# Kernel tuning notes

Hardware: AMD Instinct MI355X
Metric: run time of the kernel (lower is better)

The kernel has to match this reference:

```python
import jax, jax.numpy as jnp
import numpy as np

N_TOTAL = 1_048_576   # total points across all clouds
B = 4096              # number of point clouds
IN_FEATURES = 4
POINT_DIMS = [4, 64, 128, 256, 256]   # point encoding: 3 Linear+LeakyReLU, then final Linear(256,256)
LATENT_DIMS = [256, 256, 256]         # latent encoding: 2 Linear+LeakyReLU
LATENT_DIM = 256


def _linear_params(key, fan_in, fan_out):
    # torch nn.Linear default init: U(-1/sqrt(fan_in), 1/sqrt(fan_in))
    k1, k2 = jax.random.split(key)
    lim = 1.0 / np.sqrt(fan_in)
    w = jax.random.uniform(k1, (fan_out, fan_in), minval=-lim, maxval=lim, dtype=jnp.float32)
    b = jax.random.uniform(k2, (fan_out,), minval=-lim, maxval=lim, dtype=jnp.float32)
    return w, b


def setup_inputs() -> dict:
    key = jax.random.key(0)
    keys = jax.random.split(key, 16)
    inp = {}
    inp["points"] = jax.random.normal(keys[0], (N_TOTAL, IN_FEATURES), dtype=jnp.float32)
    # cumulative segment ends; even partition so no segment is empty (avg 256 pts/cloud)
    inp["idx"] = (jnp.arange(1, B + 1, dtype=jnp.int32) * N_TOTAL) // B
    # point encoding params
    inp["pw0"], inp["pb0"] = _linear_params(keys[1], POINT_DIMS[0], POINT_DIMS[1])
    inp["pw1"], inp["pb1"] = _linear_params(keys[2], POINT_DIMS[1], POINT_DIMS[2])
    inp["pw2"], inp["pb2"] = _linear_params(keys[3], POINT_DIMS[2], POINT_DIMS[3])
    inp["pw3"], inp["pb3"] = _linear_params(keys[4], POINT_DIMS[3], POINT_DIMS[4])
    # latent encoding params
    inp["lw0"], inp["lb0"] = _linear_params(keys[5], LATENT_DIMS[0], LATENT_DIMS[1])
    inp["lw1"], inp["lb1"] = _linear_params(keys[6], LATENT_DIMS[1], LATENT_DIMS[2])
    # mu / logvar heads
    inp["mw"], inp["mb"] = _linear_params(keys[7], LATENT_DIMS[2], LATENT_DIM)
    inp["vw"], inp["vb"] = _linear_params(keys[8], LATENT_DIMS[2], LATENT_DIM)
    return inp


def reference(points, idx, pw0, pb0, pw1, pb1, pw2, pb2, pw3, pb3,
              lw0, lb0, lw1, lb1, mw, mb, vw, vb):
    lrelu = jax.nn.leaky_relu  # default negative_slope=0.01, same as torch LeakyReLU
    h = lrelu(points @ pw0.T + pb0)
    h = lrelu(h @ pw1.T + pb1)
    h = lrelu(h @ pw2.T + pb2)
    h = h @ pw3.T + pb3                          # [N, 256]
    n = h.shape[0]
    b = idx.shape[0]
    # segment id of each point: i s.t. idx[i-1] <= j < idx[i]
    seg = jnp.searchsorted(idx, jnp.arange(n, dtype=idx.dtype), side="right")
    sums = jax.ops.segment_sum(h, seg, num_segments=b)            # [B, 256]
    counts = idx - jnp.concatenate([jnp.zeros((1,), idx.dtype), idx[:-1]])
    latent = sums / counts[:, None].astype(h.dtype)               # per-cloud mean
    # latent encoding
    latent = lrelu(latent @ lw0.T + lb0)
    latent = lrelu(latent @ lw1.T + lb1)
    mu = latent @ mw.T + mb
    log_var = latent @ vw.T + vb
    return mu, log_var
```

## Files before the change

### kernel.cpp

```cpp
#include <hip/hip_runtime.h>


#define NB    4096
#define NTOT  1048576
#define PTS   64
#define OUT_HALF (NB * 256)
#define WSPLIT_ELEMS 106496

typedef __attribute__((ext_vector_type(8))) short short8;
typedef __attribute__((ext_vector_type(4))) float f32x4;
typedef unsigned short u16;
typedef unsigned int   u32;

__device__ __forceinline__ float lrelu(float x){ return x > 0.0f ? x : 0.01f * x; }

__device__ __forceinline__ u16 f2bf(float x){
  union{float f; u32 u;} v; v.f = x;
  u32 r = v.u + 0x7fffu + ((v.u >> 16) & 1u);
  return (u16)(r >> 16);
}
__device__ __forceinline__ float bf2f(u16 h){
  union{u32 u; float f;} v; v.u = ((u32)h) << 16; return v.f;
}

__device__ __forceinline__ int find_cloud(const int* __restrict__ idx, int j){
  int lo = 0, hi = NB;
  while (lo < hi){
    int mid = (lo + hi) >> 1;
    if (idx[mid] <= j) lo = mid + 1; else hi = mid;
  }
  return lo;
}

__global__ void wsplit_kernel(const float* __restrict__ w1,
                              const float* __restrict__ w2,
                              const float* __restrict__ w3,
                              u16* __restrict__ Whi, u16* __restrict__ Wlo){
  const int tid = blockIdx.x * 256 + threadIdx.x;
  const float* W; int K, off;
  if (tid < 8192)       { W = w1; K = 64;  off = 0; }
  else if (tid < 40960) { W = w2; K = 128; off = 8192; }
  else                  { W = w3; K = 256; off = 40960; }
  const int t      = tid - off;
  const int fragId = t >> 9;
  const int r      = t & 511;
  const int lane   = r >> 3, e = r & 7;
  const int KS     = K / 32;
  const int ks     = fragId % KS, mtg = fragId / KS;
  const int m      = mtg * 16 + (lane & 15);
  const int k      = ks * 32 + (lane >> 4) * 8 + e;
  const float v = W[(size_t)m * K + k];
  const u16 hi = f2bf(v);
  const u16 lo = f2bf(v - bf2f(hi));
  Whi[tid] = hi; Wlo[tid] = lo;
}

template<int K, int M, int LDSKI, int LDSKO, bool WRITE>
__device__ __forceinline__ void mfma_layer(
    const u16* __restrict__ hin, u16* __restrict__ hout,
    const u16* __restrict__ Whi, const u16* __restrict__ Wlo,
    const float* __restrict__ bias, int w, int lane, f32x4 (*__restrict__ accRet)[4])
{
  constexpr int KS  = K / 32;
  constexpr int MTW = M / 64;
  const int lrow = lane & 15;
  const int g    = lane >> 4;

  f32x4 acc[4][MTW];
  #pragma unroll
  for (int mt = 0; mt < MTW; ++mt){
    const float bv = bias[(w * MTW + mt) * 16 + lrow];
    #pragma unroll
    for (int a = 0; a < 4; ++a){
      acc[a][mt][0] = bv; acc[a][mt][1] = bv; acc[a][mt][2] = bv; acc[a][mt][3] = bv;
    }
  }
  #pragma unroll
  for (int ks = 0; ks < KS; ++ks){
    const int eoff = ks * 32 + g * 8;
    short8 af[4];
    #pragma unroll
    for (int a = 0; a < 4; ++a)
      af[a] = *reinterpret_cast<const short8*>(hin + (a * 16 + lrow) * LDSKI + eoff);
    #pragma unroll
    for (int mt = 0; mt < MTW; ++mt){
      const int fragId = (w * MTW + mt) * KS + ks;
      const short8 bh = *reinterpret_cast<const short8*>(Whi + fragId * 512 + lane * 8);
      const short8 bl = *reinterpret_cast<const short8*>(Wlo + fragId * 512 + lane * 8);
      #pragma unroll
      for (int a = 0; a < 4; ++a)
        acc[a][mt] = __builtin_amdgcn_mfma_f32_16x16x32_bf16(af[a], bh, acc[a][mt], 0, 0, 0);
      #pragma unroll
      for (int a = 0; a < 4; ++a)
        acc[a][mt] = __builtin_amdgcn_mfma_f32_16x16x32_bf16(af[a], bl, acc[a][mt], 0, 0, 0);
    }
  }
  if constexpr (WRITE){
    #pragma unroll
    for (int a = 0; a < 4; ++a)
      #pragma unroll
      for (int mt = 0; mt < MTW; ++mt){
        const int m = (w * MTW + mt) * 16 + lrow;
        #pragma unroll
        for (int r = 0; r < 4; ++r){
          const int pt = a * 16 + g * 4 + r;
          hout[pt * LDSKO + m] = f2bf(lrelu(acc[a][mt][r]));
        }
      }
  } else {
    #pragma unroll
    for (int a = 0; a < 4; ++a)
      #pragma unroll
      for (int mt = 0; mt < MTW; ++mt)
        accRet[a][mt] = acc[a][mt];
  }
}

__global__ __launch_bounds__(256, 2)
void point_mfma_kernel(const float* __restrict__ points, const int* __restrict__ idx,
    const float* __restrict__ w0, const float* __restrict__ b0,
    const float* __restrict__ b1, const float* __restrict__ b2,
    const float* __restrict__ b3,
    const u16* __restrict__ Whi, const u16* __restrict__ Wlo,
    float* __restrict__ sums)
{
  __shared__ u16 h1[PTS][72];
  __shared__ u16 h2[PTS][136];
  __shared__ u16 h3[PTS][264];

  const int t    = threadIdx.x;
  const int base = blockIdx.x * PTS;
  const int w    = t >> 6;
  const int lane = t & 63;

  {
    const int pt  = t & 63;
    const int grp = t >> 6;
    const float4 pv = *reinterpret_cast<const float4*>(points + (size_t)(base + pt) * 4);
    #pragma unroll
    for (int j = 0; j < 16; ++j){
      const int m = grp * 16 + j;
      const float4 wv = *reinterpret_cast<const float4*>(w0 + m * 4);
      const float s = b0[m] + pv.x * wv.x + pv.y * wv.y + pv.z * wv.z + pv.w * wv.w;
      h1[pt][m] = f2bf(lrelu(s));
    }
  }
  __syncthreads();
  mfma_layer< 64, 128,  72, 136, true >(&h1[0][0], &h2[0][0], Whi + 0,     Wlo + 0,     b1, w, lane, nullptr);
  __syncthreads();
  mfma_layer<128, 256, 136, 264, true >(&h2[0][0], &h3[0][0], Whi + 8192,  Wlo + 8192,  b2, w, lane, nullptr);
  __syncthreads();
  f32x4 acc3[4][4];
  mfma_layer<256, 256, 264,   1, false>(&h3[0][0], nullptr,   Whi + 40960, Wlo + 40960, b3, w, lane, acc3);

  const int lrow = lane & 15;
  const int cF = find_cloud(idx, base);
  const int cL = find_cloud(idx, base + PTS - 1);
  if (cF == cL){
    #pragma unroll
    for (int mt = 0; mt < 4; ++mt){
      float s = 0.0f;
      #pragma unroll
      for (int a = 0; a < 4; ++a){
        const f32x4 v = acc3[a][mt];
        s += v[0] + v[1] + v[2] + v[3];
      }
      s += __shfl_xor(s, 16, 64);
      s += __shfl_xor(s, 32, 64);
      if (lane < 16)
        atomicAdd(sums + (size_t)cF * 256 + (w * 4 + mt) * 16 + lrow, s);
    }
  } else {
    const int g = lane >> 4;
    #pragma unroll
    for (int a = 0; a < 4; ++a)
      #pragma unroll
      for (int mt = 0; mt < 4; ++mt)
        #pragma unroll
        for (int r = 0; r < 4; ++r){
          const int pt = base + a * 16 + g * 4 + r;
          const int c  = find_cloud(idx, pt);
          atomicAdd(sums + (size_t)c * 256 + (w * 4 + mt) * 16 + lrow, acc3[a][mt][r]);
        }
  }
}

__device__ __forceinline__ void lat_accum(const float (*__restrict__ in)[256],
    const float* __restrict__ W, const float* __restrict__ bias, int t, float acc[4])
{
  const float bv = bias[t];
  #pragma unroll
  for (int cl = 0; cl < 4; ++cl) acc[cl] = bv;
  const float4* __restrict__ wrow = reinterpret_cast<const float4*>(W + (size_t)t * 256);
  #pragma unroll 4
  for (int k4 = 0; k4 < 64; ++k4){
    const float4 w = wrow[k4];
    #pragma unroll
    for (int cl = 0; cl < 4; ++cl){
      const float4 a = *reinterpret_cast<const float4*>(&in[cl][k4 * 4]);
      acc[cl] += a.x * w.x + a.y * w.y + a.z * w.z + a.w * w.w;
    }
  }
}

__global__ __launch_bounds__(256)
void latent_kernel(const float* __restrict__ sums, const int* __restrict__ idx,
    const float* __restrict__ lw0, const float* __restrict__ lb0,
    const float* __restrict__ lw1, const float* __restrict__ lb1,
    const float* __restrict__ mw, const float* __restrict__ mb,
    const float* __restrict__ vw, const float* __restrict__ vb,
    float* __restrict__ out)
{
  __shared__ float s_in[4][256];
  __shared__ float s_a[4][256];
  const int t  = threadIdx.x;
  const int c0 = blockIdx.x * 4;

  #pragma unroll
  for (int cl = 0; cl < 4; ++cl){
    const int c = c0 + cl;
    const int cnt = idx[c] - (c ? idx[c - 1] : 0);
    s_in[cl][t] = sums[(size_t)c * 256 + t] / (float)cnt;
  }
  __syncthreads();

  float acc[4];
  lat_accum(s_in, lw0, lb0, t, acc);
  #pragma unroll
  for (int cl = 0; cl < 4; ++cl) s_a[cl][t] = lrelu(acc[cl]);
  __syncthreads();

  lat_accum(s_a, lw1, lb1, t, acc);
  __syncthreads();
  #pragma unroll
  for (int cl = 0; cl < 4; ++cl) s_in[cl][t] = lrelu(acc[cl]);
  __syncthreads();

  float accm[4], accv[4];
  lat_accum(s_in, mw, mb, t, accm);
  lat_accum(s_in, vw, vb, t, accv);
  #pragma unroll
  for (int cl = 0; cl < 4; ++cl){
    out[(size_t)(c0 + cl) * 256 + t]                    = accm[cl];
    out[(size_t)OUT_HALF + (size_t)(c0 + cl) * 256 + t] = accv[cl];
  }
}

extern "C" void kernel_launch(void* const* d_in, const int* in_sizes, int n_in,
                              void* d_out, int out_size, void* d_ws, size_t ws_size,
                              hipStream_t stream) {
  const float* points = (const float*)d_in[0];
  const int*   idx    = (const int*)  d_in[1];
  const float* pw0 = (const float*)d_in[2],  *pb0 = (const float*)d_in[3];
  const float* pw1 = (const float*)d_in[4],  *pb1 = (const float*)d_in[5];
  const float* pw2 = (const float*)d_in[6],  *pb2 = (const float*)d_in[7];
  const float* pw3 = (const float*)d_in[8],  *pb3 = (const float*)d_in[9];
  const float* lw0 = (const float*)d_in[10], *lb0 = (const float*)d_in[11];
  const float* lw1 = (const float*)d_in[12], *lb1 = (const float*)d_in[13];
  const float* mw  = (const float*)d_in[14], *mb  = (const float*)d_in[15];
  const float* vw  = (const float*)d_in[16], *vb  = (const float*)d_in[17];
  float* out  = (float*)d_out;

  const size_t sums_bytes = (size_t)NB * 256 * sizeof(float);
  const size_t wsplit_bytes = (size_t)WSPLIT_ELEMS * 2;
  float* sums; u16* Whi; u16* Wlo;
  if (ws_size >= sums_bytes + 2 * wsplit_bytes){
    sums = (float*)d_ws;
    Whi  = (u16*)((char*)d_ws + sums_bytes);
    Wlo  = Whi + WSPLIT_ELEMS;
  } else {
    Whi  = (u16*)d_out;
    Wlo  = Whi + WSPLIT_ELEMS;
    sums = out + OUT_HALF;
  }

  hipMemsetAsync(sums, 0, sums_bytes, stream);
  wsplit_kernel<<<WSPLIT_ELEMS / 256, 256, 0, stream>>>(pw1, pw2, pw3, Whi, Wlo);
  point_mfma_kernel<<<NTOT / PTS, 256, 0, stream>>>(points, idx,
      pw0, pb0, pb1, pb2, pb3, Whi, Wlo, sums);
  latent_kernel<<<NB / 4, 256, 0, stream>>>(sums, idx,
      lw0, lb0, lw1, lb1, mw, mb, vw, vb, out);
}
```

Measured before the change: 1.166 ms.

## Alias LDS buffers, batch weight loads, raise occupancy, widen latent blocks

The point kernel now overlays the h1 and h3 LDS buffers in one shared array and raises its launch-bounds minimum from 2 to 3 blocks per CU, aiming to cut LDS and register pressure so more blocks stay resident. The MFMA inner loop is reordered to loop over output tiles first and to load up to four hi/lo weight fragments at once before issuing the MFMAs, which hides global-load latency. The latent kernel handles 16 clouds per block instead of 4, so each weight row is read once for four times as many clouds. The risks are register spills under the tighter launch bound, activation fragments now being reloaded from LDS once per output tile, and fewer latent blocks to spread across the GPU.

Result: faster. 1.084 ms (-7.1%).

```diff
diff --git a/kernel.cpp b/kernel.cpp
--- a/kernel.cpp
+++ b/kernel.cpp
@@ -51,8 +51,8 @@
   const int k      = ks * 32 + (lane >> 4) * 8 + e;
   const float v = W[(size_t)m * K + k];
   const u16 hi = f2bf(v);
-  const u16 lo = f2bf(v - bf2f(hi));
-  Whi[tid] = hi; Wlo[tid] = lo;
+  Whi[tid] = hi;
+  Wlo[tid] = f2bf(v - bf2f(hi));
 }
 
 template<int K, int M, int LDSKI, int LDSKO, bool WRITE>
@@ -63,6 +63,7 @@
 {
   constexpr int KS  = K / 32;
   constexpr int MTW = M / 64;
+  constexpr int KC  = (KS < 4) ? KS : 4;
   const int lrow = lane & 15;
   const int g    = lane >> 4;
 
@@ -75,26 +76,38 @@
       acc[a][mt][0] = bv; acc[a][mt][1] = bv; acc[a][mt][2] = bv; acc[a][mt][3] = bv;
     }
   }
-  #pragma unroll
-  for (int ks = 0; ks < KS; ++ks){
-    const int eoff = ks * 32 + g * 8;
-    short8 af[4];
-    #pragma unroll
-    for (int a = 0; a < 4; ++a)
-      af[a] = *reinterpret_cast<const short8*>(hin + (a * 16 + lrow) * LDSKI + eoff);
-    #pragma unroll
-    for (int mt = 0; mt < MTW; ++mt){
-      const int fragId = (w * MTW + mt) * KS + ks;
-      const short8 bh = *reinterpret_cast<const short8*>(Whi + fragId * 512 + lane * 8);
-      const short8 bl = *reinterpret_cast<const short8*>(Wlo + fragId * 512 + lane * 8);
-      #pragma unroll
-      for (int a = 0; a < 4; ++a)
-        acc[a][mt] = __builtin_amdgcn_mfma_f32_16x16x32_bf16(af[a], bh, acc[a][mt], 0, 0, 0);
-      #pragma unroll
-      for (int a = 0; a < 4; ++a)
-        acc[a][mt] = __builtin_amdgcn_mfma_f32_16x16x32_bf16(af[a], bl, acc[a][mt], 0, 0, 0);
-    }
-  }
+
+  const u16* __restrict__ bptr = Whi + (size_t)(w * MTW) * KS * 512 + lane * 8;
+  const u16* __restrict__ lptr = Wlo + (size_t)(w * MTW) * KS * 512 + lane * 8;
+
+  #pragma unroll
+  for (int mt = 0; mt < MTW; ++mt){
+    #pragma unroll
+    for (int kc = 0; kc < KS; kc += KC){
+      short8 bh[KC], bl[KC];
+      #pragma unroll
+      for (int i = 0; i < KC; ++i){
+        bh[i] = *reinterpret_cast<const short8*>(bptr + (size_t)(mt * KS + kc + i) * 512);
+        bl[i] = *reinterpret_cast<const short8*>(lptr + (size_t)(mt * KS + kc + i) * 512);
+      }
+      #pragma unroll
+      for (int i = 0; i < KC; ++i){
+        const int ks = kc + i;
+        short8 af[4];
+        const int eoff = ks * 32 + g * 8;
+        #pragma unroll
+        for (int a = 0; a < 4; ++a)
+          af[a] = *reinterpret_cast<const short8*>(hin + (a * 16 + lrow) * LDSKI + eoff);
+        #pragma unroll
+        for (int a = 0; a < 4; ++a)
+          acc[a][mt] = __builtin_amdgcn_mfma_f32_16x16x32_bf16(af[a], bh[i], acc[a][mt], 0, 0, 0);
+        #pragma unroll
+        for (int a = 0; a < 4; ++a)
+          acc[a][mt] = __builtin_amdgcn_mfma_f32_16x16x32_bf16(af[a], bl[i], acc[a][mt], 0, 0, 0);
+      }
+    }
+  }
+
   if constexpr (WRITE){
     #pragma unroll
     for (int a = 0; a < 4; ++a)
@@ -116,7 +129,7 @@
   }
 }
 
-__global__ __launch_bounds__(256, 2)
+__global__ __launch_bounds__(256, 3)
 void point_mfma_kernel(const float* __restrict__ points, const int* __restrict__ idx,
     const float* __restrict__ w0, const float* __restrict__ b0,
     const float* __restrict__ b1, const float* __restrict__ b2,
@@ -124,9 +137,10 @@
     const u16* __restrict__ Whi, const u16* __restrict__ Wlo,
     float* __restrict__ sums)
 {
-  __shared__ u16 h1[PTS][72];
-  __shared__ u16 h2[PTS][136];
-  __shared__ u16 h3[PTS][264];
+  __shared__ __align__(16) char smem[51200];
+  u16 (*h2)[136] = reinterpret_cast<u16(*)[136]>(smem);
+  u16 (*h1)[72]  = reinterpret_cast<u16(*)[72]>(smem + 17408);
+  u16 (*h3)[264] = reinterpret_cast<u16(*)[264]>(smem + 17408);
 
   const int t    = threadIdx.x;
   const int base = blockIdx.x * PTS;
@@ -185,18 +199,19 @@
   }
 }
 
+#define CPB 16
 __device__ __forceinline__ void lat_accum(const float (*__restrict__ in)[256],
-    const float* __restrict__ W, const float* __restrict__ bias, int t, float acc[4])
+    const float* __restrict__ W, const float* __restrict__ bias, int t, float* acc)
 {
   const float bv = bias[t];
   #pragma unroll
-  for (int cl = 0; cl < 4; ++cl) acc[cl] = bv;
+  for (int cl = 0; cl < CPB; ++cl) acc[cl] = bv;
   const float4* __restrict__ wrow = reinterpret_cast<const float4*>(W + (size_t)t * 256);
   #pragma unroll 4
   for (int k4 = 0; k4 < 64; ++k4){
     const float4 w = wrow[k4];
     #pragma unroll
-    for (int cl = 0; cl < 4; ++cl){
+    for (int cl = 0; cl < CPB; ++cl){
       const float4 a = *reinterpret_cast<const float4*>(&in[cl][k4 * 4]);
       acc[cl] += a.x * w.x + a.y * w.y + a.z * w.z + a.w * w.w;
     }
@@ -211,36 +226,36 @@
     const float* __restrict__ vw, const float* __restrict__ vb,
     float* __restrict__ out)
 {
-  __shared__ float s_in[4][256];
-  __shared__ float s_a[4][256];
+  __shared__ float s_in[CPB][256];
+  __shared__ float s_a[CPB][256];
   const int t  = threadIdx.x;
-  const int c0 = blockIdx.x * 4;
-
-  #pragma unroll
-  for (int cl = 0; cl < 4; ++cl){
+  const int c0 = blockIdx.x * CPB;
+
+  #pragma unroll
+  for (int cl = 0; cl < CPB; ++cl){
     const int c = c0 + cl;
     const int cnt = idx[c] - (c ? idx[c - 1] : 0);
     s_in[cl][t] = sums[(size_t)c * 256 + t] / (float)cnt;
   }
   __syncthreads();
 
-  float acc[4];
+  float acc[CPB];
   lat_accum(s_in, lw0, lb0, t, acc);
   #pragma unroll
-  for (int cl = 0; cl < 4; ++cl) s_a[cl][t] = lrelu(acc[cl]);
+  for (int cl = 0; cl < CPB; ++cl) s_a[cl][t] = lrelu(acc[cl]);
   __syncthreads();
 
   lat_accum(s_a, lw1, lb1, t, acc);
   __syncthreads();
   #pragma unroll
-  for (int cl = 0; cl < 4; ++cl) s_in[cl][t] = lrelu(acc[cl]);
-  __syncthreads();
-
-  float accm[4], accv[4];
+  for (int cl = 0; cl < CPB; ++cl) s_in[cl][t] = lrelu(acc[cl]);
+  __syncthreads();
+
+  float accm[CPB], accv[CPB];
   lat_accum(s_in, mw, mb, t, accm);
   lat_accum(s_in, vw, vb, t, accv);
   #pragma unroll
-  for (int cl = 0; cl < 4; ++cl){
+  for (int cl = 0; cl < CPB; ++cl){
     out[(size_t)(c0 + cl) * 256 + t]                    = accm[cl];
     out[(size_t)OUT_HALF + (size_t)(c0 + cl) * 256 + t] = accv[cl];
   }
@@ -278,6 +293,6 @@
   wsplit_kernel<<<WSPLIT_ELEMS / 256, 256, 0, stream>>>(pw1, pw2, pw3, Whi, Wlo);
   point_mfma_kernel<<<NTOT / PTS, 256, 0, stream>>>(points, idx,
       pw0, pb0, pb1, pb2, pb3, Whi, Wlo, sums);
-  latent_kernel<<<NB / 4, 256, 0, stream>>>(sums, idx,
+  latent_kernel<<<NB / CPB, 256, 0, stream>>>(sums, idx,
       lw0, lb0, lw1, lb1, mw, mb, vw, vb, out);
 }
```
